# Optimization experiments

Measured on AMD Instinct MI355X. Metric: run time of the kernel, lower is better.

Reference implementation:

```python
import jax, jax.numpy as jnp
import numpy as np
from jax import lax

B, DF, DO, DK, DV, KER, STR = 32, 2048, 2048, 128, 128, 4, 2
STR_Q = int(np.ceil(DF / DO))  # = 1, so query conv has kernel=stride=1


def conv1d(x, w, stride):
    # x: [B, Cin, L], w: [Cout, Cin, K] -> [B, Cout, Lout], VALID, no bias
    return lax.conv_general_dilated(x, w, (stride,), 'VALID',
                                    dimension_numbers=('NCH', 'OIH', 'NCH'))


def layernorm(x, w, b, eps):
    m = jnp.mean(x, axis=-1, keepdims=True)
    v = jnp.mean(jnp.square(x - m), axis=-1, keepdims=True)
    return (x - m) * lax.rsqrt(v + eps) * w + b


def setup_inputs() -> dict:
    key = jax.random.key(0)
    ks = jax.random.split(key, 10)
    s = 0.02
    return {
        'features': jax.random.normal(ks[0], (B, DF), dtype=jnp.float32),
        'shuffled_index': jax.random.randint(ks[1], (DF,), 0, DF, dtype=jnp.int32),
        'ln_w': jnp.ones((DF,), jnp.float32),
        'ln_b': jnp.zeros((DF,), jnp.float32),
        'q_w': jax.random.normal(ks[2], (DK, 1, STR_Q), jnp.float32) * s,
        'k_w': jax.random.normal(ks[3], (DK, 1, KER), jnp.float32) * s,
        'v_w': jax.random.normal(ks[4], (DV, 1, KER), jnp.float32) * s,
        'conv_w': jax.random.normal(ks[5], (1, DV, 1), jnp.float32) * s,
        'bn_ln_w': jnp.ones((DO,), jnp.float32),
        'bn_ln_b': jnp.zeros((DO,), jnp.float32),
        'w1_w': jax.random.normal(ks[6], (DO, DO), jnp.float32) * s,
        'w1_b': jnp.zeros((DO,), jnp.float32),
        'w2_w': jax.random.normal(ks[7], (DO, DO), jnp.float32) * s,
        'w2_b': jnp.zeros((DO,), jnp.float32),
    }


def reference(features, shuffled_index, ln_w, ln_b, q_w, k_w, v_w, conv_w,
              bn_ln_w, bn_ln_b, w1_w, w1_b, w2_w, w2_b):
    residual = features                               # [B, DF]
    q_in = layernorm(features, ln_w, ln_b, 1e-5)[:, None, :]   # [B,1,DF]
    shuf = features[:, shuffled_index][:, None, :]             # [B,1,DF]

    query = conv1d(q_in, q_w, STR_Q)                  # [B, DK, DO]
    key_t = conv1d(shuf, k_w, STR)                    # [B, DK, NC]
    value = conv1d(shuf, v_w, STR)                    # [B, DV, NC]

    # ScaledDotProduction, temperature=1, dropout eval-mode identity
    attn = jnp.einsum('bkq,bkc->bqc', query, key_t)   # [B, DO, NC]
    attn = jax.nn.softmax(attn, axis=2)
    out = jnp.einsum('bqc,bvc->bqv', attn, value)     # [B, DO, DV]

    # output Conv1d(d_v -> 1, kernel 1) applied to [B, DV, DO]
    out = jnp.einsum('bqv,v->bq', out, conv_w[0, :, 0])  # [B, DO]
    out = out + residual                              # d_features == d_out

    # Bottleneck FFN
    r = out
    h = layernorm(out, bn_ln_w, bn_ln_b, 1e-6)
    h = jax.nn.relu(h @ w1_w.T + w1_b) @ w2_w.T + w2_b
    out = h + r
    return (out, attn)
```

## Files before the change

### kernel.cpp

```cpp
#include <hip/hip_runtime.h>
#include <float.h>

#define NB 32
#define D  2048
#define NC 1023
#define RPB 8

typedef float f32x4 __attribute__((ext_vector_type(4)));

#define OFF_LN   0
#define OFF_SW   (NB*D)
#define OFF_MM   (OFF_SW + 2*NB*NC)
#define OFF_OUT1 (OFF_MM + 64)
#define OFF_LN2  (OFF_OUT1 + NB*D)
#define OFF_H    (OFF_LN2 + NB*D)

__device__ __forceinline__ float wred_sum(float x){
  #pragma unroll
  for (int o = 32; o; o >>= 1) x += __shfl_xor(x, o);
  return x;
}

__global__ __launch_bounds__(256) void prep_kernel(
    const float* __restrict__ feat, const int* __restrict__ idx,
    const float* __restrict__ ln_w, const float* __restrict__ ln_b,
    const float* __restrict__ q_w,  const float* __restrict__ k_w,
    const float* __restrict__ v_w,  const float* __restrict__ conv_w,
    float* __restrict__ ws)
{
  __shared__ float sh_feat[D];
  __shared__ float sh_shuf[D];
  __shared__ float red_s[4][2];
  __shared__ float red_k[4][8];
  __shared__ float red_mm[4][2];

  const int b = blockIdx.x;
  const int t = threadIdx.x;
  const int wid = t >> 6;

  const float4* fb4 = (const float4*)(feat + b * D);
  float4* sf4 = (float4*)sh_feat;
  float4 fv[2];
  float s1 = 0.f, s2 = 0.f;
  #pragma unroll
  for (int j = 0; j < 2; ++j) {
    float4 v = fb4[t + j * 256];
    fv[j] = v;
    sf4[t + j * 256] = v;
    s1 += (v.x + v.y) + (v.z + v.w);
    s2 += fmaf(v.x, v.x, fmaf(v.y, v.y, fmaf(v.z, v.z, v.w * v.w)));
  }

  float pk[4] = {0,0,0,0}, pv[4] = {0,0,0,0};
  if (t < 128) {
    float qv = q_w[t], cv = conv_w[t];
    #pragma unroll
    for (int j = 0; j < 4; ++j) {
      pk[j] = qv * k_w[t * 4 + j];
      pv[j] = cv * v_w[t * 4 + j];
    }
  }
  s1 = wred_sum(s1); s2 = wred_sum(s2);
  #pragma unroll
  for (int j = 0; j < 4; ++j) { pk[j] = wred_sum(pk[j]); pv[j] = wred_sum(pv[j]); }
  if ((t & 63) == 0) {
    red_s[wid][0] = s1; red_s[wid][1] = s2;
    #pragma unroll
    for (int j = 0; j < 4; ++j) { red_k[wid][j] = pk[j]; red_k[wid][4 + j] = pv[j]; }
  }
  __syncthreads();

  const float S1 = red_s[0][0] + red_s[1][0] + red_s[2][0] + red_s[3][0];
  const float S2 = red_s[0][1] + red_s[1][1] + red_s[2][1] + red_s[3][1];
  float kq[4], vw[4];
  #pragma unroll
  for (int j = 0; j < 4; ++j) {
    kq[j] = red_k[0][j] + red_k[1][j] + red_k[2][j] + red_k[3][j];
    vw[j] = red_k[0][4+j] + red_k[1][4+j] + red_k[2][4+j] + red_k[3][4+j];
  }
  const float mean = S1 * (1.f / D);
  const float rstd = rsqrtf(S2 * (1.f / D) - mean * mean + 1e-5f);

  float* lnp = ws + OFF_LN + b * D;
  const float4* lw4 = (const float4*)ln_w;
  const float4* lb4 = (const float4*)ln_b;
  #pragma unroll
  for (int j = 0; j < 2; ++j) {
    int i = t + j * 256;
    float4 v = fv[j], w = lw4[i], bb = lb4[i], o;
    o.x = (v.x - mean) * rstd * w.x + bb.x;
    o.y = (v.y - mean) * rstd * w.y + bb.y;
    o.z = (v.z - mean) * rstd * w.z + bb.z;
    o.w = (v.w - mean) * rstd * w.w + bb.w;
    ((float4*)lnp)[i] = o;
  }

  #pragma unroll
  for (int j = 0; j < 8; ++j) {
    int i = t + j * 256;
    sh_shuf[i] = sh_feat[idx[i]];
  }
  __syncthreads();

  float2* swp = (float2*)(ws + OFF_SW) + b * NC;
  float lmax = -FLT_MAX, lmin = FLT_MAX;
  #pragma unroll
  for (int j = 0; j < 4; ++j) {
    int c = t + j * 256;
    if (c < NC) {
      float a0 = sh_shuf[2*c], a1 = sh_shuf[2*c+1], a2 = sh_shuf[2*c+2], a3 = sh_shuf[2*c+3];
      float sv = fmaf(a0, kq[0], fmaf(a1, kq[1], fmaf(a2, kq[2], a3 * kq[3])));
      float wv = fmaf(a0, vw[0], fmaf(a1, vw[1], fmaf(a2, vw[2], a3 * vw[3])));
      float2 p; p.x = sv; p.y = wv;
      swp[c] = p;
      lmax = fmaxf(lmax, sv);
      lmin = fminf(lmin, sv);
    }
  }
  #pragma unroll
  for (int o = 32; o; o >>= 1) {
    lmax = fmaxf(lmax, __shfl_xor(lmax, o));
    lmin = fminf(lmin, __shfl_xor(lmin, o));
  }
  if ((t & 63) == 0) { red_mm[wid][0] = lmax; red_mm[wid][1] = lmin; }
  __syncthreads();
  if (t == 0) {
    ws[OFF_MM + b]      = fmaxf(fmaxf(red_mm[0][0], red_mm[1][0]), fmaxf(red_mm[2][0], red_mm[3][0]));
    ws[OFF_MM + NB + b] = fminf(fminf(red_mm[0][1], red_mm[1][1]), fminf(red_mm[2][1], red_mm[3][1]));
  }
}

__global__ __launch_bounds__(256) void attn_kernel(
    const float* __restrict__ feat, float* __restrict__ ws,
    float* __restrict__ out)
{
  __shared__ float ebuf[RPB * 1024];
  __shared__ float2 sws[1024];
  __shared__ float sinv[RPB];

  const int row0 = blockIdx.x * RPB;
  const int b = row0 >> 11;
  const int t = threadIdx.x;
  const int wid = t >> 6, lane = t & 63;

  const float smax = ws[OFF_MM + b], smin = ws[OFF_MM + NB + b];
  const float2* swg = (const float2*)(ws + OFF_SW) + b * NC;
  #pragma unroll
  for (int j = 0; j < 4; ++j) {
    int c = t + j * 256;
    if (c < NC) sws[c] = swg[c];
  }
  __syncthreads();

  #pragma unroll
  for (int rr = 0; rr < 2; ++rr) {
    const int r = wid * 2 + rr;
    const int row = row0 + r;
    const float alpha = ws[OFF_LN + row];
    const float m = (alpha >= 0.f) ? alpha * smax : alpha * smin;
    float* eb = ebuf + r * NC;
    float l = 0.f, acc = 0.f;
    #pragma unroll
    for (int j = 0; j < 16; ++j) {
      int c = lane + j * 64;
      if (c < NC) {
        float2 p = sws[c];
        float e = __expf(fmaf(alpha, p.x, -m));
        eb[c] = e;
        l += e;
        acc = fmaf(e, p.y, acc);
      }
    }
    #pragma unroll
    for (int o = 32; o; o >>= 1) { l += __shfl_xor(l, o); acc += __shfl_xor(acc, o); }
    if (lane == 0) {
      float inv = 1.f / l;
      sinv[r] = inv;
      ws[OFF_OUT1 + row] = fmaf(acc, inv, feat[row]);
    }
  }
  __syncthreads();

  f32x4* base = (f32x4*)(out + NB * D + (size_t)row0 * NC);
  const f32x4* eb4 = (const f32x4*)ebuf;
  #pragma unroll
  for (int j = 0; j < 8; ++j) {
    int i4 = t + j * 256;
    if (i4 < 2046) {
      f32x4 v = eb4[i4];
      int g = i4 * 4;
      int r0 = g / NC, r1 = (g + 1) / NC, r2 = (g + 2) / NC, r3 = (g + 3) / NC;
      v.x *= sinv[r0]; v.y *= sinv[r1]; v.z *= sinv[r2]; v.w *= sinv[r3];
      __builtin_nontemporal_store(v, base + i4);
    }
  }
}

__global__ __launch_bounds__(256) void ln2_init_kernel(
    const float* __restrict__ bnw, const float* __restrict__ bnb,
    const float* __restrict__ w1b, const float* __restrict__ w2b,
    float* __restrict__ ws, float* __restrict__ out)
{
  __shared__ float red_s[4][2];
  const int b = blockIdx.x, t = threadIdx.x;
  const int wid = t >> 6;
  const float4* x4 = (const float4*)(ws + OFF_OUT1 + b * D);
  float4 xv[2];
  float s1 = 0.f, s2 = 0.f;
  #pragma unroll
  for (int j = 0; j < 2; ++j) {
    float4 v = x4[t + j * 256];
    xv[j] = v;
    s1 += (v.x + v.y) + (v.z + v.w);
    s2 += fmaf(v.x, v.x, fmaf(v.y, v.y, fmaf(v.z, v.z, v.w * v.w)));
  }
  s1 = wred_sum(s1); s2 = wred_sum(s2);
  if ((t & 63) == 0) { red_s[wid][0] = s1; red_s[wid][1] = s2; }
  __syncthreads();
  const float S1 = red_s[0][0] + red_s[1][0] + red_s[2][0] + red_s[3][0];
  const float S2 = red_s[0][1] + red_s[1][1] + red_s[2][1] + red_s[3][1];
  const float mean = S1 * (1.f / D);
  const float rstd = rsqrtf(S2 * (1.f / D) - mean * mean + 1e-6f);

  float4* ln2p = (float4*)(ws + OFF_LN2 + b * D);
  float4* hp   = (float4*)(ws + OFF_H   + b * D);
  float4* op   = (float4*)out + b * (D / 4);
  const float4* bw4 = (const float4*)bnw;
  const float4* bb4 = (const float4*)bnb;
  const float4* w1b4 = (const float4*)w1b;
  const float4* w2b4 = (const float4*)w2b;
  #pragma unroll
  for (int j = 0; j < 2; ++j) {
    int i = t + j * 256;
    float4 v = xv[j], w = bw4[i], bb = bb4[i], o;
    o.x = (v.x - mean) * rstd * w.x + bb.x;
    o.y = (v.y - mean) * rstd * w.y + bb.y;
    o.z = (v.z - mean) * rstd * w.z + bb.z;
    o.w = (v.w - mean) * rstd * w.w + bb.w;
    ln2p[i] = o;
    hp[i] = w1b4[i];
    float4 w2 = w2b4[i], oo;
    oo.x = v.x + w2.x; oo.y = v.y + w2.y; oo.z = v.z + w2.z; oo.w = v.w + w2.w;
    op[i] = oo;
  }
}

template<int RELU>
__global__ __launch_bounds__(128) void gemm_kernel(
    const float* __restrict__ X, const float* __restrict__ W,
    float* __restrict__ out)
{
  __shared__ float xs[32][132];
  __shared__ float wtT[128 * 64];
  const int nb = blockIdx.x & 31;
  const int kb = blockIdx.x >> 5;
  const int n0 = nb * 64;
  const int k0 = kb * 128;
  const int t = threadIdx.x;
  const int tm = t >> 4;
  const int tn = t & 15;

  #pragma unroll
  for (int jj = 0; jj < 8; ++jj) {
    int idx = jj * 128 + t;
    int m_r = idx >> 5, q_r = idx & 31;
    float4 v = *(const float4*)(X + m_r * 2048 + k0 + q_r * 4);
    if (RELU) {
      v.x = fmaxf(v.x, 0.f); v.y = fmaxf(v.y, 0.f);
      v.z = fmaxf(v.z, 0.f); v.w = fmaxf(v.w, 0.f);
    }
    *(float4*)(&xs[m_r][q_r * 4]) = v;
  }
  #pragma unroll
  for (int jj = 0; jj < 16; ++jj) {
    int idx = jj * 128 + t;
    int n_r = idx >> 5, q_r = idx & 31;
    float4 v = *(const float4*)(W + (n0 + n_r) * 2048 + k0 + q_r * 4);
    float vv[4] = {v.x, v.y, v.z, v.w};
    #pragma unroll
    for (int c = 0; c < 4; ++c) {
      int kk = q_r * 4 + c;
      wtT[kk * 64 + ((((n_r >> 2) ^ (kk & 15)) << 2) | (n_r & 3))] = vv[c];
    }
  }
  __syncthreads();

  float4 acc0 = {0,0,0,0}, acc1 = {0,0,0,0}, acc2 = {0,0,0,0}, acc3 = {0,0,0,0};
  #pragma unroll 2
  for (int kq = 0; kq < 32; ++kq) {
    float4 xq0 = *(const float4*)(&xs[tm * 4 + 0][kq * 4]);
    float4 xq1 = *(const float4*)(&xs[tm * 4 + 1][kq * 4]);
    float4 xq2 = *(const float4*)(&xs[tm * 4 + 2][kq * 4]);
    float4 xq3 = *(const float4*)(&xs[tm * 4 + 3][kq * 4]);
    #pragma unroll
    for (int c = 0; c < 4; ++c) {
      int kk = kq * 4 + c;
      float4 wv = *(const float4*)(&wtT[kk * 64 + ((tn ^ (kk & 15)) << 2)]);
      float x0 = (c==0)?xq0.x:(c==1)?xq0.y:(c==2)?xq0.z:xq0.w;
      float x1 = (c==0)?xq1.x:(c==1)?xq1.y:(c==2)?xq1.z:xq1.w;
      float x2 = (c==0)?xq2.x:(c==1)?xq2.y:(c==2)?xq2.z:xq2.w;
      float x3 = (c==0)?xq3.x:(c==1)?xq3.y:(c==2)?xq3.z:xq3.w;
      acc0.x = fmaf(x0, wv.x, acc0.x); acc0.y = fmaf(x0, wv.y, acc0.y);
      acc0.z = fmaf(x0, wv.z, acc0.z); acc0.w = fmaf(x0, wv.w, acc0.w);
      acc1.x = fmaf(x1, wv.x, acc1.x); acc1.y = fmaf(x1, wv.y, acc1.y);
      acc1.z = fmaf(x1, wv.z, acc1.z); acc1.w = fmaf(x1, wv.w, acc1.w);
      acc2.x = fmaf(x2, wv.x, acc2.x); acc2.y = fmaf(x2, wv.y, acc2.y);
      acc2.z = fmaf(x2, wv.z, acc2.z); acc2.w = fmaf(x2, wv.w, acc2.w);
      acc3.x = fmaf(x3, wv.x, acc3.x); acc3.y = fmaf(x3, wv.y, acc3.y);
      acc3.z = fmaf(x3, wv.z, acc3.z); acc3.w = fmaf(x3, wv.w, acc3.w);
    }
  }

  float* op0 = out + (tm * 4 + 0) * 2048 + n0 + tn * 4;
  float* op1 = op0 + 2048;
  float* op2 = op1 + 2048;
  float* op3 = op2 + 2048;
  atomicAdd(op0+0, acc0.x); atomicAdd(op0+1, acc0.y); atomicAdd(op0+2, acc0.z); atomicAdd(op0+3, acc0.w);
  atomicAdd(op1+0, acc1.x); atomicAdd(op1+1, acc1.y); atomicAdd(op1+2, acc1.z); atomicAdd(op1+3, acc1.w);
  atomicAdd(op2+0, acc2.x); atomicAdd(op2+1, acc2.y); atomicAdd(op2+2, acc2.z); atomicAdd(op2+3, acc2.w);
  atomicAdd(op3+0, acc3.x); atomicAdd(op3+1, acc3.y); atomicAdd(op3+2, acc3.z); atomicAdd(op3+3, acc3.w);
}

extern "C" void kernel_launch(void* const* d_in, const int* in_sizes, int n_in,
                              void* d_out, int out_size, void* d_ws, size_t ws_size,
                              hipStream_t stream)
{
  (void)in_sizes; (void)n_in; (void)out_size; (void)ws_size;
  const float* feat   = (const float*)d_in[0];
  const int*   idx    = (const int*)d_in[1];
  const float* ln_w   = (const float*)d_in[2];
  const float* ln_b   = (const float*)d_in[3];
  const float* q_w    = (const float*)d_in[4];
  const float* k_w    = (const float*)d_in[5];
  const float* v_w    = (const float*)d_in[6];
  const float* conv_w = (const float*)d_in[7];
  const float* bnw    = (const float*)d_in[8];
  const float* bnb    = (const float*)d_in[9];
  const float* w1w    = (const float*)d_in[10];
  const float* w1b    = (const float*)d_in[11];
  const float* w2w    = (const float*)d_in[12];
  const float* w2b    = (const float*)d_in[13];
  float* out = (float*)d_out;
  float* ws  = (float*)d_ws;

  prep_kernel<<<dim3(NB), dim3(256), 0, stream>>>(feat, idx, ln_w, ln_b, q_w, k_w, v_w, conv_w, ws);
  attn_kernel<<<dim3(NB * D / RPB), dim3(256), 0, stream>>>(feat, ws, out);
  ln2_init_kernel<<<dim3(NB), dim3(256), 0, stream>>>(bnw, bnb, w1b, w2b, ws, out);
  gemm_kernel<0><<<dim3(512), dim3(128), 0, stream>>>(ws + OFF_LN2, w1w, ws + OFF_H);
  gemm_kernel<1><<<dim3(512), dim3(128), 0, stream>>>(ws + OFF_H, w2w, out);
}
```

Before: 374.8 us.

## Replace split-K atomic accumulation with partial buffers and separate reduction kernels

```diff
diff --git a/kernel.cpp b/kernel.cpp
--- a/kernel.cpp
+++ b/kernel.cpp
@@ -14,6 +14,7 @@
 #define OFF_OUT1 (OFF_MM + 64)
 #define OFF_LN2  (OFF_OUT1 + NB*D)
 #define OFF_H    (OFF_LN2 + NB*D)
+#define OFF_P    (OFF_H + NB*D)
 
 __device__ __forceinline__ float wred_sum(float x){
   #pragma unroll
@@ -189,17 +190,21 @@
     if (i4 < 2046) {
       f32x4 v = eb4[i4];
       int g = i4 * 4;
-      int r0 = g / NC, r1 = (g + 1) / NC, r2 = (g + 2) / NC, r3 = (g + 3) / NC;
-      v.x *= sinv[r0]; v.y *= sinv[r1]; v.z *= sinv[r2]; v.w *= sinv[r3];
+      int r0 = g / NC;
+      int rem = g - r0 * NC;
+      float i0 = sinv[r0];
+      float i1 = sinv[r0 + (rem >= NC - 1)];
+      float i2 = sinv[r0 + (rem >= NC - 2)];
+      float i3 = sinv[r0 + (rem >= NC - 3)];
+      v.x *= i0; v.y *= i1; v.z *= i2; v.w *= i3;
       __builtin_nontemporal_store(v, base + i4);
     }
   }
 }
 
-__global__ __launch_bounds__(256) void ln2_init_kernel(
+__global__ __launch_bounds__(256) void ln2_kernel(
     const float* __restrict__ bnw, const float* __restrict__ bnb,
-    const float* __restrict__ w1b, const float* __restrict__ w2b,
-    float* __restrict__ ws, float* __restrict__ out)
+    float* __restrict__ ws)
 {
   __shared__ float red_s[4][2];
   const int b = blockIdx.x, t = threadIdx.x;
@@ -223,12 +228,8 @@
   const float rstd = rsqrtf(S2 * (1.f / D) - mean * mean + 1e-6f);
 
   float4* ln2p = (float4*)(ws + OFF_LN2 + b * D);
-  float4* hp   = (float4*)(ws + OFF_H   + b * D);
-  float4* op   = (float4*)out + b * (D / 4);
   const float4* bw4 = (const float4*)bnw;
   const float4* bb4 = (const float4*)bnb;
-  const float4* w1b4 = (const float4*)w1b;
-  const float4* w2b4 = (const float4*)w2b;
   #pragma unroll
   for (int j = 0; j < 2; ++j) {
     int i = t + j * 256;
@@ -238,17 +239,12 @@
     o.z = (v.z - mean) * rstd * w.z + bb.z;
     o.w = (v.w - mean) * rstd * w.w + bb.w;
     ln2p[i] = o;
-    hp[i] = w1b4[i];
-    float4 w2 = w2b4[i], oo;
-    oo.x = v.x + w2.x; oo.y = v.y + w2.y; oo.z = v.z + w2.z; oo.w = v.w + w2.w;
-    op[i] = oo;
-  }
-}
-
-template<int RELU>
+  }
+}
+
 __global__ __launch_bounds__(128) void gemm_kernel(
     const float* __restrict__ X, const float* __restrict__ W,
-    float* __restrict__ out)
+    float* __restrict__ P)
 {
   __shared__ float xs[32][132];
   __shared__ float wtT[128 * 64];
@@ -265,10 +261,6 @@
     int idx = jj * 128 + t;
     int m_r = idx >> 5, q_r = idx & 31;
     float4 v = *(const float4*)(X + m_r * 2048 + k0 + q_r * 4);
-    if (RELU) {
-      v.x = fmaxf(v.x, 0.f); v.y = fmaxf(v.y, 0.f);
-      v.z = fmaxf(v.z, 0.f); v.w = fmaxf(v.w, 0.f);
-    }
     *(float4*)(&xs[m_r][q_r * 4]) = v;
   }
   #pragma unroll
@@ -311,14 +303,49 @@
     }
   }
 
-  float* op0 = out + (tm * 4 + 0) * 2048 + n0 + tn * 4;
-  float* op1 = op0 + 2048;
-  float* op2 = op1 + 2048;
-  float* op3 = op2 + 2048;
-  atomicAdd(op0+0, acc0.x); atomicAdd(op0+1, acc0.y); atomicAdd(op0+2, acc0.z); atomicAdd(op0+3, acc0.w);
-  atomicAdd(op1+0, acc1.x); atomicAdd(op1+1, acc1.y); atomicAdd(op1+2, acc1.z); atomicAdd(op1+3, acc1.w);
-  atomicAdd(op2+0, acc2.x); atomicAdd(op2+1, acc2.y); atomicAdd(op2+2, acc2.z); atomicAdd(op2+3, acc2.w);
-  atomicAdd(op3+0, acc3.x); atomicAdd(op3+1, acc3.y); atomicAdd(op3+2, acc3.z); atomicAdd(op3+3, acc3.w);
+  float* p0 = P + kb * (NB * D) + (tm * 4 + 0) * 2048 + n0 + tn * 4;
+  *(float4*)(p0)          = acc0;
+  *(float4*)(p0 + 2048)   = acc1;
+  *(float4*)(p0 + 4096)   = acc2;
+  *(float4*)(p0 + 6144)   = acc3;
+}
+
+__global__ __launch_bounds__(256) void reduce_h_kernel(
+    const float* __restrict__ ws_in, const float* __restrict__ w1b,
+    float* __restrict__ ws_out)
+{
+  const int i4 = blockIdx.x * 256 + threadIdx.x;
+  const float4* P4 = (const float4*)(ws_in + OFF_P);
+  float4 a = P4[i4];
+  #pragma unroll
+  for (int kb = 1; kb < 16; ++kb) {
+    float4 p = P4[kb * 16384 + i4];
+    a.x += p.x; a.y += p.y; a.z += p.z; a.w += p.w;
+  }
+  float4 bb = ((const float4*)w1b)[i4 & 511];
+  a.x = fmaxf(a.x + bb.x, 0.f);
+  a.y = fmaxf(a.y + bb.y, 0.f);
+  a.z = fmaxf(a.z + bb.z, 0.f);
+  a.w = fmaxf(a.w + bb.w, 0.f);
+  ((float4*)(ws_out + OFF_H))[i4] = a;
+}
+
+__global__ __launch_bounds__(256) void reduce_out_kernel(
+    const float* __restrict__ ws_in, const float* __restrict__ w2b,
+    float* __restrict__ out)
+{
+  const int i4 = blockIdx.x * 256 + threadIdx.x;
+  const float4* P4 = (const float4*)(ws_in + OFF_P);
+  float4 a = P4[i4];
+  #pragma unroll
+  for (int kb = 1; kb < 16; ++kb) {
+    float4 p = P4[kb * 16384 + i4];
+    a.x += p.x; a.y += p.y; a.z += p.z; a.w += p.w;
+  }
+  float4 bb = ((const float4*)w2b)[i4 & 511];
+  float4 r  = ((const float4*)(ws_in + OFF_OUT1))[i4];
+  a.x += bb.x + r.x; a.y += bb.y + r.y; a.z += bb.z + r.z; a.w += bb.w + r.w;
+  ((float4*)out)[i4] = a;
 }
 
 extern "C" void kernel_launch(void* const* d_in, const int* in_sizes, int n_in,
@@ -345,7 +372,9 @@
 
   prep_kernel<<<dim3(NB), dim3(256), 0, stream>>>(feat, idx, ln_w, ln_b, q_w, k_w, v_w, conv_w, ws);
   attn_kernel<<<dim3(NB * D / RPB), dim3(256), 0, stream>>>(feat, ws, out);
-  ln2_init_kernel<<<dim3(NB), dim3(256), 0, stream>>>(bnw, bnb, w1b, w2b, ws, out);
-  gemm_kernel<0><<<dim3(512), dim3(128), 0, stream>>>(ws + OFF_LN2, w1w, ws + OFF_H);
-  gemm_kernel<1><<<dim3(512), dim3(128), 0, stream>>>(ws + OFF_H, w2w, out);
-}
+  ln2_kernel<<<dim3(NB), dim3(256), 0, stream>>>(bnw, bnb, ws);
+  gemm_kernel<<<dim3(512), dim3(128), 0, stream>>>(ws + OFF_LN2, w1w, ws + OFF_P);
+  reduce_h_kernel<<<dim3(64), dim3(256), 0, stream>>>(ws, w1b, ws);
+  gemm_kernel<<<dim3(512), dim3(128), 0, stream>>>(ws + OFF_H, w2w, ws + OFF_P);
+  reduce_out_kernel<<<dim3(64), dim3(256), 0, stream>>>(ws, w2b, out);
+}
```

Result: faster. 359.9 us (-4.0%).
